# Optimization experiments

Hardware: AMD Instinct MI355X
Metric: run time of the kernel (lower is better)

## Reference

```python
import jax, jax.numpy as jnp
import numpy as np

D, H, C = 128, 256, 10
SEQ, BATCH = 2048, 64


def _lstm_layer(x, Wih, Whh, b):
    """PyTorch-style LSTM layer. x: [S,B,Din], Wih: [4H,Din], Whh: [4H,H], b: [4H].
    Gate order i,f,g,o. Returns hidden sequence [S,B,H]."""
    # precompute input projections for all timesteps at once
    xw = jnp.einsum('sbd,gd->sbg', x, Wih) + b  # [S,B,4H]
    h0 = jnp.zeros((x.shape[1], Whh.shape[1]), x.dtype)
    c0 = jnp.zeros_like(h0)

    def step(carry, xw_t):
        h, c = carry
        gates = xw_t + h @ Whh.T  # [B,4H]
        i, f, g, o = jnp.split(gates, 4, axis=-1)
        i = jax.nn.sigmoid(i)
        f = jax.nn.sigmoid(f)
        g = jnp.tanh(g)
        o = jax.nn.sigmoid(o)
        c = f * c + i * g
        h = o * jnp.tanh(c)
        return (h, c), h

    _, hs = jax.lax.scan(step, (h0, c0), xw)
    return hs  # [S,B,H]


def setup_inputs() -> dict:
    key = jax.random.key(0)
    ks = jax.random.split(key, 8)
    s1 = 1.0 / np.sqrt(H)
    x = jax.random.normal(ks[0], (SEQ, BATCH, D), jnp.float32)
    Wih1 = jax.random.uniform(ks[1], (4 * H, D), jnp.float32, -s1, s1)
    Whh1 = jax.random.uniform(ks[2], (4 * H, H), jnp.float32, -s1, s1)
    b1 = jax.random.uniform(ks[3], (4 * H,), jnp.float32, -s1, s1)  # b_ih + b_hh folded
    Wih2 = jax.random.uniform(ks[4], (4 * H, H), jnp.float32, -s1, s1)
    Whh2 = jax.random.uniform(ks[5], (4 * H, H), jnp.float32, -s1, s1)
    b2 = jax.random.uniform(ks[6], (4 * H,), jnp.float32, -s1, s1)
    Wlin = jax.random.uniform(ks[7], (C, H), jnp.float32, -s1, s1)
    blin = jnp.zeros((C,), jnp.float32)
    return {"x": x, "Wih1": Wih1, "Whh1": Whh1, "b1": b1,
            "Wih2": Wih2, "Whh2": Whh2, "b2": b2,
            "Wlin": Wlin, "blin": blin}


def reference(x, Wih1, Whh1, b1, Wih2, Whh2, b2, Wlin, blin):
    h1 = jnp.tanh(_lstm_layer(x, Wih1, Whh1, b1))          # [S,B,H]
    h2 = jnp.tanh(_lstm_layer(h1, Wih2, Whh2, b2))         # [S,B,H]
    # squeeze() is a no-op for S>1, B>1
    out = jax.nn.sigmoid(jnp.einsum('sbh,ch->sbc', h2, Wlin) + blin)  # [S,B,C]
    return out
```

## Files before the change

kernel.cpp:

```cpp
#include <hip/hip_runtime.h>

typedef _Float16 half8 __attribute__((ext_vector_type(8)));
typedef float    f32x4 __attribute__((ext_vector_type(4)));

static constexpr int S_ = 2048;
static constexpr int B_ = 64;
static constexpr int D_ = 128;
static constexpr int H_ = 256;
static constexpr int C_ = 10;

static constexpr int NBLK = 64;
static constexpr int NTHR = 512;
static constexpr int HHALF = B_ * H_;

__device__ __attribute__((aligned(64))) unsigned g_f[NBLK * 16];

#define LD_AG(p)    __hip_atomic_load((p), __ATOMIC_RELAXED, __HIP_MEMORY_SCOPE_AGENT)
#define ST_AG(p, v) __hip_atomic_store((p), (v), __ATOMIC_RELAXED, __HIP_MEMORY_SCOPE_AGENT)

__device__ __forceinline__ float fs(float v) { return 1.0f / (1.0f + __expf(-v)); }
__device__ __forceinline__ float ft(float v) { return 1.0f - 2.0f / (__expf(2.0f * v) + 1.0f); }

__device__ __forceinline__ half8 ldh16(const _Float16* p) {
    union { double d[2]; half8 h; } u;
    u.d[0] = LD_AG((const double*)p);
    u.d[1] = LD_AG(((const double*)p) + 1);
    return u.h;
}

__device__ __forceinline__ void ldg16x8(half8* r,
    const _Float16* p0, const _Float16* p1, const _Float16* p2, const _Float16* p3,
    const _Float16* p4, const _Float16* p5, const _Float16* p6, const _Float16* p7)
{
    asm volatile(
        "global_load_dwordx4 %0, %8, off sc0 sc1\n\t"
        "global_load_dwordx4 %1, %9, off sc0 sc1\n\t"
        "global_load_dwordx4 %2, %10, off sc0 sc1\n\t"
        "global_load_dwordx4 %3, %11, off sc0 sc1\n\t"
        "global_load_dwordx4 %4, %12, off sc0 sc1\n\t"
        "global_load_dwordx4 %5, %13, off sc0 sc1\n\t"
        "global_load_dwordx4 %6, %14, off sc0 sc1\n\t"
        "global_load_dwordx4 %7, %15, off sc0 sc1\n\t"
        "s_waitcnt vmcnt(0)"
        : "=&v"(r[0]), "=&v"(r[1]), "=&v"(r[2]), "=&v"(r[3]),
          "=&v"(r[4]), "=&v"(r[5]), "=&v"(r[6]), "=&v"(r[7])
        : "v"(p0), "v"(p1), "v"(p2), "v"(p3),
          "v"(p4), "v"(p5), "v"(p6), "v"(p7)
        : "memory");
}

__device__ __forceinline__ void ldg16x8x2(half8* r,
                                          const _Float16* pa, const _Float16* pb)
{
    const _Float16* a0 = pa + 2048;  const _Float16* a1 = pa + 6144;
    const _Float16* a2 = pa + 10240; const _Float16* a3 = pa + 14336;
    const _Float16* b0 = pb + 2048;  const _Float16* b1 = pb + 6144;
    const _Float16* b2 = pb + 10240; const _Float16* b3 = pb + 14336;
    asm volatile(
        "global_load_dwordx4 %0, %16, off offset:-4096 sc0 sc1\n\t"
        "global_load_dwordx4 %1, %16, off sc0 sc1\n\t"
        "global_load_dwordx4 %2, %17, off offset:-4096 sc0 sc1\n\t"
        "global_load_dwordx4 %3, %17, off sc0 sc1\n\t"
        "global_load_dwordx4 %4, %18, off offset:-4096 sc0 sc1\n\t"
        "global_load_dwordx4 %5, %18, off sc0 sc1\n\t"
        "global_load_dwordx4 %6, %19, off offset:-4096 sc0 sc1\n\t"
        "global_load_dwordx4 %7, %19, off sc0 sc1\n\t"
        "global_load_dwordx4 %8, %20, off offset:-4096 sc0 sc1\n\t"
        "global_load_dwordx4 %9, %20, off sc0 sc1\n\t"
        "global_load_dwordx4 %10, %21, off offset:-4096 sc0 sc1\n\t"
        "global_load_dwordx4 %11, %21, off sc0 sc1\n\t"
        "global_load_dwordx4 %12, %22, off offset:-4096 sc0 sc1\n\t"
        "global_load_dwordx4 %13, %22, off sc0 sc1\n\t"
        "global_load_dwordx4 %14, %23, off offset:-4096 sc0 sc1\n\t"
        "global_load_dwordx4 %15, %23, off sc0 sc1\n\t"
        "s_waitcnt vmcnt(0)"
        : "=&v"(r[0]),  "=&v"(r[1]),  "=&v"(r[2]),  "=&v"(r[3]),
          "=&v"(r[4]),  "=&v"(r[5]),  "=&v"(r[6]),  "=&v"(r[7]),
          "=&v"(r[8]),  "=&v"(r[9]),  "=&v"(r[10]), "=&v"(r[11]),
          "=&v"(r[12]), "=&v"(r[13]), "=&v"(r[14]), "=&v"(r[15])
        : "v"(a0), "v"(a1), "v"(a2), "v"(a3),
          "v"(b0), "v"(b1), "v"(b2), "v"(b3)
        : "memory");
}

__device__ __forceinline__ void stg16(_Float16* p, half8 v) {
    asm volatile("global_store_dwordx4 %0, %1, off sc0 sc1"
                 :: "v"(p), "v"(v) : "memory");
}

__device__ __forceinline__ half8 cvt8(float4 a, float4 b) {
    half8 r;
    r[0] = (_Float16)a.x; r[1] = (_Float16)a.y; r[2] = (_Float16)a.z; r[3] = (_Float16)a.w;
    r[4] = (_Float16)b.x; r[5] = (_Float16)b.y; r[6] = (_Float16)b.z; r[7] = (_Float16)b.w;
    return r;
}

__global__ __launch_bounds__(NTHR, 1)
void lstm2_ef(const float* __restrict__ x,
              const float* __restrict__ Wih1, const float* __restrict__ Whh1,
              const float* __restrict__ b1,
              const float* __restrict__ Wih2, const float* __restrict__ Whh2,
              const float* __restrict__ b2,
              const float* __restrict__ Wlin, const float* __restrict__ blin,
              float* __restrict__ out, _Float16* __restrict__ hb)
{
    const int bid = blockIdx.x, tid = threadIdx.x;
    const bool isL2 = (bid >= 32);
    const int blk  = bid & 31;
    const int lane = tid & 63, w = tid >> 6;
    const int mt   = w & 3;
    const int nt   = w >> 2;
    const int n    = lane & 15;
    const int kg   = lane >> 4;
    const int c4   = n >> 2, gate = n & 3;
    const int lc   = nt * 4 + c4;
    const int col  = blk * 8 + lc;
    const int rowg = gate * H_ + col;
    const int batchA = mt * 16 + n;

    _Float16* h1raw = hb;
    _Float16* h1t   = hb + 3 * HHALF;
    _Float16* h2raw = hb + 6 * HHALF;
    _Float16* h2t   = hb + 9 * HHALF;

    __shared__ __align__(16) _Float16 sh[2][B_][8];

    const unsigned base = LD_AG(&g_f[bid * 16]);

    { double* z = (double*)hb;
      for (int i = bid * NTHR + tid; i < 49152; i += NBLK * NTHR) ST_AG(z + i, 0.0); }

    half8 bfrag[16];
    if (!isL2) {
        #pragma unroll
        for (int kt = 0; kt < 4; ++kt) {
            const float* p = Wih1 + (size_t)rowg * D_ + kt * 32 + kg * 8;
            bfrag[kt] = cvt8(*(const float4*)p, *(const float4*)(p + 4));
        }
        #pragma unroll
        for (int kt = 4; kt < 12; ++kt) {
            const float* p = Whh1 + (size_t)rowg * H_ + (kt - 4) * 32 + kg * 8;
            bfrag[kt] = cvt8(*(const float4*)p, *(const float4*)(p + 4));
        }
    } else {
        #pragma unroll
        for (int kt = 0; kt < 8; ++kt) {
            const float* p = Wih2 + (size_t)rowg * H_ + kt * 32 + kg * 8;
            bfrag[kt] = cvt8(*(const float4*)p, *(const float4*)(p + 4));
        }
        #pragma unroll
        for (int kt = 8; kt < 16; ++kt) {
            const float* p = Whh2 + (size_t)rowg * H_ + (kt - 8) * 32 + kg * 8;
            bfrag[kt] = cvt8(*(const float4*)p, *(const float4*)(p + 4));
        }
    }
    const float bias_n = isL2 ? b2[rowg] : b1[rowg];

    __syncthreads();
    if (tid == 0) ST_AG(&g_f[bid * 16], base + 1u);

    float cr[4] = {0.f, 0.f, 0.f, 0.f};

    float4 xf[8];
    if (!isL2) {
        const float* xr = x + (size_t)batchA * D_;
        #pragma unroll
        for (int q = 0; q < 4; ++q) {
            xf[2 * q]     = *(const float4*)(xr + q * 32 + kg * 8);
            xf[2 * q + 1] = *(const float4*)(xr + q * 32 + kg * 8 + 4);
        }
    }

    int w3 = 0;

    for (int t = 0; t <= S_ + 1; ++t) {
        const int r1 = (w3 == 0) ? 2 : w3 - 1;
        const int r2 = (w3 == 2) ? 0 : w3 + 1;

        {
            const unsigned et1 = base + (unsigned)t + 1u;
            if (tid < 64) {
                const unsigned tg = (tid < 32 || isL2 || t == 0) ? et1 : et1 - 1u;
                while ((int)(LD_AG(&g_f[tid * 16]) - tg) < 0)
                    __builtin_amdgcn_s_sleep(1);
            }
            __syncthreads();
        }

        if (!isL2) {
            if (t < S_) {
                half8 af[12];
                {
                    af[0] = cvt8(xf[0], xf[1]);
                    af[1] = cvt8(xf[2], xf[3]);
                    af[2] = cvt8(xf[4], xf[5]);
                    af[3] = cvt8(xf[6], xf[7]);
                }
                const _Float16* hp = h1raw + r1 * HHALF + (((size_t)kg * 64 + batchA) << 3);
                ldg16x8(&af[4], hp,          hp + 2048,  hp + 4096,  hp + 6144,
                                hp + 8192,   hp + 10240, hp + 12288, hp + 14336);
                f32x4 accA = {0.f, 0.f, 0.f, 0.f}, accB = {0.f, 0.f, 0.f, 0.f};
                #pragma unroll
                for (int kt = 0; kt < 12; kt += 2) {
                    accA = __builtin_amdgcn_mfma_f32_16x16x32_f16(af[kt],     bfrag[kt],     accA, 0, 0, 0);
                    accB = __builtin_amdgcn_mfma_f32_16x16x32_f16(af[kt + 1], bfrag[kt + 1], accB, 0, 0, 0);
                }
                #pragma unroll
                for (int r = 0; r < 4; ++r) {
                    const float pre = accA[r] + accB[r] + bias_n;
                    const float av  = (gate == 2) ? ft(pre) : fs(pre);
                    const int lb = (lane & 48) | (c4 << 2);
                    const float gi = __shfl(av, lb | 0, 64), gf = __shfl(av, lb | 1, 64);
                    const float gg = __shfl(av, lb | 2, 64), go = __shfl(av, lb | 3, 64);
                    const float cn = gf * cr[r] + gi * gg; cr[r] = cn;
                    const float hv = go * ft(cn);
                    const int bD = mt * 16 + kg * 4 + r;
                    if (gate == 0) sh[0][bD][lc] = (_Float16)hv;
                    if (gate == 1) sh[1][bD][lc] = (_Float16)ft(hv);
                }
            }
        } else {
            if (t >= 1 && t <= S_) {
                half8 af[16];
                const _Float16* h1p = h1t   + r1 * HHALF + (((size_t)kg * 64 + batchA) << 3);
                const _Float16* h2p = h2raw + r2 * HHALF + (((size_t)kg * 64 + batchA) << 3);
                ldg16x8x2(af, h1p, h2p);
                f32x4 accA = {0.f, 0.f, 0.f, 0.f}, accB = {0.f, 0.f, 0.f, 0.f};
                #pragma unroll
                for (int kt = 0; kt < 16; kt += 2) {
                    accA = __builtin_amdgcn_mfma_f32_16x16x32_f16(af[kt],     bfrag[kt],     accA, 0, 0, 0);
                    accB = __builtin_amdgcn_mfma_f32_16x16x32_f16(af[kt + 1], bfrag[kt + 1], accB, 0, 0, 0);
                }
                #pragma unroll
                for (int r = 0; r < 4; ++r) {
                    const float pre = accA[r] + accB[r] + bias_n;
                    const float av  = (gate == 2) ? ft(pre) : fs(pre);
                    const int lb = (lane & 48) | (c4 << 2);
                    const float gi = __shfl(av, lb | 0, 64), gf = __shfl(av, lb | 1, 64);
                    const float gg = __shfl(av, lb | 2, 64), go = __shfl(av, lb | 3, 64);
                    const float cn = gf * cr[r] + gi * gg; cr[r] = cn;
                    const float hv = go * ft(cn);
                    const int bD = mt * 16 + kg * 4 + r;
                    if (gate == 0) sh[0][bD][lc] = (_Float16)hv;
                    if (gate == 1) sh[1][bD][lc] = (_Float16)ft(hv);
                }
            }
        }

        __syncthreads();

        if (tid < 64) {
            const int b = tid;
            bool doit; int slot;
            if (!isL2) { doit = (t < S_);            slot = w3; }
            else       { doit = (t >= 1 && t <= S_); slot = r1; }
            if (doit) {
                const half8 s0 = *(const half8*)&sh[0][b][0];
                const half8 s1 = *(const half8*)&sh[1][b][0];
                _Float16* braw = isL2 ? h2raw : h1raw;
                _Float16* btnh = isL2 ? h2t   : h1t;
                stg16(braw + slot * HHALF + ((blk * 64 + b) << 3), s0);
                stg16(btnh + slot * HHALF + ((blk * 64 + b) << 3), s1);
            }
            asm volatile("s_waitcnt vmcnt(0)" ::: "memory");
            __builtin_amdgcn_sched_barrier(0);
            if (tid == 0) ST_AG(&g_f[bid * 16], base + (unsigned)t + 2u);
        }

        if (!isL2 && t + 1 < S_) {
            const float* xr = x + ((size_t)(t + 1) * B_ + batchA) * D_;
            #pragma unroll
            for (int q = 0; q < 4; ++q) {
                xf[2 * q]     = *(const float4*)(xr + q * 32 + kg * 8);
                xf[2 * q + 1] = *(const float4*)(xr + q * 32 + kg * 8 + 4);
            }
        }
        if (isL2 && t >= 2) {
            const int g16 = tid >> 4;
            if (g16 < 20) {
                const int dot = blk * 20 + g16, cls = dot >> 6, ob = dot & 63, l16 = tid & 15;
                const _Float16* hB = h2t + r2 * HHALF;
                const half8 v0 = ldh16(hB + (((2 * l16)     * 64 + ob) << 3));
                const half8 v1 = ldh16(hB + (((2 * l16 + 1) * 64 + ob) << 3));
                const float* wr = Wlin + (size_t)cls * H_ + l16 * 16;
                float p = 0.f;
                #pragma unroll
                for (int j = 0; j < 8; ++j) p += (float)v0[j] * wr[j] + (float)v1[j] * wr[8 + j];
                p += __shfl_xor(p, 1, 64); p += __shfl_xor(p, 2, 64);
                p += __shfl_xor(p, 4, 64); p += __shfl_xor(p, 8, 64);
                if (l16 == 0)
                    out[((size_t)(t - 2) * B_ + ob) * C_ + cls] = fs(p + blin[cls]);
            }
        }

        w3 = r2;
    }
}

extern "C" void kernel_launch(void* const* d_in, const int* in_sizes, int n_in,
                              void* d_out, int out_size, void* d_ws, size_t ws_size,
                              hipStream_t stream)
{
    const float* x    = (const float*)d_in[0];
    const float* Wih1 = (const float*)d_in[1];
    const float* Whh1 = (const float*)d_in[2];
    const float* b1   = (const float*)d_in[3];
    const float* Wih2 = (const float*)d_in[4];
    const float* Whh2 = (const float*)d_in[5];
    const float* b2   = (const float*)d_in[6];
    const float* Wlin = (const float*)d_in[7];
    const float* blin = (const float*)d_in[8];
    float* out = (float*)d_out;
    _Float16* hb = (_Float16*)d_ws;

    void* args[] = { (void*)&x, (void*)&Wih1, (void*)&Whh1, (void*)&b1,
                     (void*)&Wih2, (void*)&Whh2, (void*)&b2,
                     (void*)&Wlin, (void*)&blin, (void*)&out, (void*)&hb };
    hipLaunchCooperativeKernel((const void*)lstm2_ef, dim3(NBLK), dim3(NTHR),
                               args, 0, stream);
}
```

Baseline: 9.233 ms.

## Store LSTM hidden states straight from every wave instead of via LDS staging

Each wave now packs its four fp16 hidden values, and their tanh, into 64-bit words with lane shuffles. It writes them straight to the global exchange buffers, replacing the LDS staging area and the wave-0 copy-out step after the barrier. This removes one serialized phase from the per-timestep critical path before the step flag is published. The output-head dot products move off wave 0, and their reads use inline asm global loads instead of paired atomic loads. The risk is that the flag store now depends on __syncthreads having drained the other waves' global stores, with no explicit vmcnt wait.

New measurement: 9.980 ms. 1.08x slower.

```diff
diff --git a/kernel.cpp b/kernel.cpp
--- a/kernel.cpp
+++ b/kernel.cpp
@@ -2,6 +2,8 @@
 
 typedef _Float16 half8 __attribute__((ext_vector_type(8)));
 typedef float    f32x4 __attribute__((ext_vector_type(4)));
+typedef unsigned u32;
+typedef unsigned long long u64;
 
 static constexpr int S_ = 2048;
 static constexpr int B_ = 64;
@@ -20,13 +22,6 @@
 
 __device__ __forceinline__ float fs(float v) { return 1.0f / (1.0f + __expf(-v)); }
 __device__ __forceinline__ float ft(float v) { return 1.0f - 2.0f / (__expf(2.0f * v) + 1.0f); }
-
-__device__ __forceinline__ half8 ldh16(const _Float16* p) {
-    union { double d[2]; half8 h; } u;
-    u.d[0] = LD_AG((const double*)p);
-    u.d[1] = LD_AG(((const double*)p) + 1);
-    return u.h;
-}
 
 __device__ __forceinline__ void ldg16x8(half8* r,
     const _Float16* p0, const _Float16* p1, const _Float16* p2, const _Float16* p3,
@@ -83,9 +78,16 @@
         : "memory");
 }
 
-__device__ __forceinline__ void stg16(_Float16* p, half8 v) {
-    asm volatile("global_store_dwordx4 %0, %1, off sc0 sc1"
-                 :: "v"(p), "v"(v) : "memory");
+__device__ __forceinline__ void ldg16x2(half8* r,
+                                        const _Float16* p0, const _Float16* p1)
+{
+    asm volatile(
+        "global_load_dwordx4 %0, %2, off sc0 sc1\n\t"
+        "global_load_dwordx4 %1, %3, off sc0 sc1\n\t"
+        "s_waitcnt vmcnt(0)"
+        : "=&v"(r[0]), "=&v"(r[1])
+        : "v"(p0), "v"(p1)
+        : "memory");
 }
 
 __device__ __forceinline__ half8 cvt8(float4 a, float4 b) {
@@ -123,8 +125,6 @@
     _Float16* h2raw = hb + 6 * HHALF;
     _Float16* h2t   = hb + 9 * HHALF;
 
-    __shared__ __align__(16) _Float16 sh[2][B_][8];
-
     const unsigned base = LD_AG(&g_f[bid * 16]);
 
     { double* z = (double*)hb;
@@ -187,8 +187,12 @@
             __syncthreads();
         }
 
-        if (!isL2) {
-            if (t < S_) {
+        const bool act = isL2 ? (t >= 1 && t <= S_) : (t < S_);
+        const int slot = isL2 ? r1 : w3;
+        f32x4 accA = {0.f, 0.f, 0.f, 0.f}, accB = {0.f, 0.f, 0.f, 0.f};
+
+        if (act) {
+            if (!isL2) {
                 half8 af[12];
                 {
                     af[0] = cvt8(xf[0], xf[1]);
@@ -199,73 +203,62 @@
                 const _Float16* hp = h1raw + r1 * HHALF + (((size_t)kg * 64 + batchA) << 3);
                 ldg16x8(&af[4], hp,          hp + 2048,  hp + 4096,  hp + 6144,
                                 hp + 8192,   hp + 10240, hp + 12288, hp + 14336);
-                f32x4 accA = {0.f, 0.f, 0.f, 0.f}, accB = {0.f, 0.f, 0.f, 0.f};
                 #pragma unroll
                 for (int kt = 0; kt < 12; kt += 2) {
                     accA = __builtin_amdgcn_mfma_f32_16x16x32_f16(af[kt],     bfrag[kt],     accA, 0, 0, 0);
                     accB = __builtin_amdgcn_mfma_f32_16x16x32_f16(af[kt + 1], bfrag[kt + 1], accB, 0, 0, 0);
                 }
-                #pragma unroll
-                for (int r = 0; r < 4; ++r) {
-                    const float pre = accA[r] + accB[r] + bias_n;
-                    const float av  = (gate == 2) ? ft(pre) : fs(pre);
-                    const int lb = (lane & 48) | (c4 << 2);
-                    const float gi = __shfl(av, lb | 0, 64), gf = __shfl(av, lb | 1, 64);
-                    const float gg = __shfl(av, lb | 2, 64), go = __shfl(av, lb | 3, 64);
-                    const float cn = gf * cr[r] + gi * gg; cr[r] = cn;
-                    const float hv = go * ft(cn);
-                    const int bD = mt * 16 + kg * 4 + r;
-                    if (gate == 0) sh[0][bD][lc] = (_Float16)hv;
-                    if (gate == 1) sh[1][bD][lc] = (_Float16)ft(hv);
-                }
-            }
-        } else {
-            if (t >= 1 && t <= S_) {
+            } else {
                 half8 af[16];
                 const _Float16* h1p = h1t   + r1 * HHALF + (((size_t)kg * 64 + batchA) << 3);
                 const _Float16* h2p = h2raw + r2 * HHALF + (((size_t)kg * 64 + batchA) << 3);
                 ldg16x8x2(af, h1p, h2p);
-                f32x4 accA = {0.f, 0.f, 0.f, 0.f}, accB = {0.f, 0.f, 0.f, 0.f};
                 #pragma unroll
                 for (int kt = 0; kt < 16; kt += 2) {
                     accA = __builtin_amdgcn_mfma_f32_16x16x32_f16(af[kt],     bfrag[kt],     accA, 0, 0, 0);
                     accB = __builtin_amdgcn_mfma_f32_16x16x32_f16(af[kt + 1], bfrag[kt + 1], accB, 0, 0, 0);
                 }
-                #pragma unroll
-                for (int r = 0; r < 4; ++r) {
-                    const float pre = accA[r] + accB[r] + bias_n;
-                    const float av  = (gate == 2) ? ft(pre) : fs(pre);
-                    const int lb = (lane & 48) | (c4 << 2);
-                    const float gi = __shfl(av, lb | 0, 64), gf = __shfl(av, lb | 1, 64);
-                    const float gg = __shfl(av, lb | 2, 64), go = __shfl(av, lb | 3, 64);
-                    const float cn = gf * cr[r] + gi * gg; cr[r] = cn;
-                    const float hv = go * ft(cn);
-                    const int bD = mt * 16 + kg * 4 + r;
-                    if (gate == 0) sh[0][bD][lc] = (_Float16)hv;
-                    if (gate == 1) sh[1][bD][lc] = (_Float16)ft(hv);
+            }
+
+            _Float16* braw = isL2 ? h2raw : h1raw;
+            _Float16* btnh = isL2 ? h2t   : h1t;
+            const int qb = lane & 48;
+            #pragma unroll
+            for (int r = 0; r < 4; ++r) {
+                const float pre = accA[r] + accB[r] + bias_n;
+                const float av  = (gate == 2) ? ft(pre) : fs(pre);
+                const int lb = qb | (c4 << 2);
+                const float gi = __shfl(av, lb | 0, 64), gf = __shfl(av, lb | 1, 64);
+                const float gg = __shfl(av, lb | 2, 64), go = __shfl(av, lb | 3, 64);
+                const float cn = gf * cr[r] + gi * gg; cr[r] = cn;
+                const float hv = go * ft(cn);
+                union { _Float16 h; unsigned short s; } ch, ct;
+                ch.h = (_Float16)hv; ct.h = (_Float16)ft(hv);
+                const unsigned hr = ch.s, tr = ct.s;
+                const unsigned a0 = (unsigned)__shfl((int)hr, qb | 0,  64);
+                const unsigned a1 = (unsigned)__shfl((int)hr, qb | 4,  64);
+                const unsigned a2 = (unsigned)__shfl((int)hr, qb | 8,  64);
+                const unsigned a3 = (unsigned)__shfl((int)hr, qb | 12, 64);
+                const unsigned t0 = (unsigned)__shfl((int)tr, qb | 0,  64);
+                const unsigned t1 = (unsigned)__shfl((int)tr, qb | 4,  64);
+                const unsigned t2 = (unsigned)__shfl((int)tr, qb | 8,  64);
+                const unsigned t3 = (unsigned)__shfl((int)tr, qb | 12, 64);
+                const int bD = mt * 16 + kg * 4 + r;
+                const size_t ho = (size_t)slot * HHALF + ((blk * 64 + bD) << 3) + nt * 4;
+                if ((lane & 15) == 0) {
+                    const u64 pk = (u64)(a0 & 0xffffu) | ((u64)(a1 & 0xffffu) << 16)
+                                 | ((u64)(a2 & 0xffffu) << 32) | ((u64)(a3 & 0xffffu) << 48);
+                    ST_AG((u64*)(braw + ho), pk);
+                } else if ((lane & 15) == 1) {
+                    const u64 pk = (u64)(t0 & 0xffffu) | ((u64)(t1 & 0xffffu) << 16)
+                                 | ((u64)(t2 & 0xffffu) << 32) | ((u64)(t3 & 0xffffu) << 48);
+                    ST_AG((u64*)(btnh + ho), pk);
                 }
             }
         }
 
         __syncthreads();
-
-        if (tid < 64) {
-            const int b = tid;
-            bool doit; int slot;
-            if (!isL2) { doit = (t < S_);            slot = w3; }
-            else       { doit = (t >= 1 && t <= S_); slot = r1; }
-            if (doit) {
-                const half8 s0 = *(const half8*)&sh[0][b][0];
-                const half8 s1 = *(const half8*)&sh[1][b][0];
-                _Float16* braw = isL2 ? h2raw : h1raw;
-                _Float16* btnh = isL2 ? h2t   : h1t;
-                stg16(braw + slot * HHALF + ((blk * 64 + b) << 3), s0);
-                stg16(btnh + slot * HHALF + ((blk * 64 + b) << 3), s1);
-            }
-            asm volatile("s_waitcnt vmcnt(0)" ::: "memory");
-            __builtin_amdgcn_sched_barrier(0);
-            if (tid == 0) ST_AG(&g_f[bid * 16], base + (unsigned)t + 2u);
-        }
+        if (tid == 0) ST_AG(&g_f[bid * 16], base + (unsigned)t + 2u);
 
         if (!isL2 && t + 1 < S_) {
             const float* xr = x + ((size_t)(t + 1) * B_ + batchA) * D_;
@@ -276,16 +269,17 @@
             }
         }
         if (isL2 && t >= 2) {
-            const int g16 = tid >> 4;
-            if (g16 < 20) {
-                const int dot = blk * 20 + g16, cls = dot >> 6, ob = dot & 63, l16 = tid & 15;
+            const int hg = (tid >> 4) - 4;
+            if (hg >= 0 && hg < 20) {
+                const int dot = blk * 20 + hg, cls = dot >> 6, ob = dot & 63, l16 = tid & 15;
                 const _Float16* hB = h2t + r2 * HHALF;
-                const half8 v0 = ldh16(hB + (((2 * l16)     * 64 + ob) << 3));
-                const half8 v1 = ldh16(hB + (((2 * l16 + 1) * 64 + ob) << 3));
+                half8 v[2];
+                ldg16x2(v, hB + (((2 * l16)     * 64 + ob) << 3),
+                           hB + (((2 * l16 + 1) * 64 + ob) << 3));
                 const float* wr = Wlin + (size_t)cls * H_ + l16 * 16;
                 float p = 0.f;
                 #pragma unroll
-                for (int j = 0; j < 8; ++j) p += (float)v0[j] * wr[j] + (float)v1[j] * wr[8 + j];
+                for (int j = 0; j < 8; ++j) p += (float)v[0][j] * wr[j] + (float)v[1][j] * wr[8 + j];
                 p += __shfl_xor(p, 1, 64); p += __shfl_xor(p, 2, 64);
                 p += __shfl_xor(p, 4, 64); p += __shfl_xor(p, 8, 64);
                 if (l16 == 0)
```
